# Kernel tuning notes

Hardware: AMD Instinct MI355X
Metric: run time of the kernel (lower is better)

The kernel has to match this reference:

```python
import jax, jax.numpy as jnp
import numpy as np

N_NODES = 100000
N_EDGES = 3200000
F_IN = 256
HEADS = 8
C_OUT = 8
NEG_SLOPE = 0.2


def setup_inputs() -> dict:
    key = jax.random.key(0)
    k1, k2, k3, k4, k5, k6 = jax.random.split(key, 6)
    x = jax.random.normal(k1, (N_NODES, F_IN), dtype=jnp.float32)
    edge_index = jax.random.randint(k2, (2, N_EDGES), 0, N_NODES, dtype=jnp.int64)
    W = jax.random.normal(k3, (F_IN, HEADS * C_OUT), dtype=jnp.float32) * (1.0 / np.sqrt(F_IN))
    att_src = jax.random.normal(k4, (HEADS, C_OUT), dtype=jnp.float32) * 0.1
    att_dst = jax.random.normal(k5, (HEADS, C_OUT), dtype=jnp.float32) * 0.1
    bias = jax.random.normal(k6, (HEADS * C_OUT,), dtype=jnp.float32) * 0.01
    return {"x": x, "edge_index": edge_index, "W": W, "att_src": att_src, "att_dst": att_dst, "bias": bias}


def reference(x, edge_index, W, att_src, att_dst, bias):
    # GATConv (PyG semantics), concat=True, inference (dropout off).
    N = x.shape[0]
    H, C = att_src.shape
    h = (x @ W).reshape(N, H, C)                      # [N,H,C] transformed features
    a_src = jnp.einsum('nhc,hc->nh', h, att_src)      # [N,H]
    a_dst = jnp.einsum('nhc,hc->nh', h, att_dst)      # [N,H]
    src, dst = edge_index[0], edge_index[1]
    # per-edge raw attention logits
    e = jax.nn.leaky_relu(a_src[src] + a_dst[dst], NEG_SLOPE)  # [E,H]
    # segment softmax over incoming edges of each destination node
    m = jax.ops.segment_max(e, dst, num_segments=N)            # [N,H]
    e = jnp.exp(e - m[dst])
    s = jax.ops.segment_sum(e, dst, num_segments=N)            # [N,H]
    alpha = e / (s[dst] + 1e-16)                               # [E,H]
    # scatter-add weighted neighbor features
    out = jax.ops.segment_sum(alpha[:, :, None] * h[src], dst, num_segments=N)  # [N,H,C]
    return out.reshape(N, H * C) + bias
```

## Files before the change

kernel.cpp:

```cpp
#include <hip/hip_runtime.h>
#include <hip/hip_fp16.h>
#include <math.h>

#define F_IN 256
#define HC 64
#define NHEAD 8
#define NEG 0.2f
#define BSH 7
#define BSZ 128
#define CAP 5376
#define HCAP 2944

typedef __attribute__((ext_vector_type(8))) short bf16x8;
typedef __attribute__((ext_vector_type(4))) float f32x4;

union BV { uint4 q; bf16x8 v; };

__device__ __forceinline__ unsigned int hi_pair(float a, float b) {
  return __builtin_amdgcn_perm(__float_as_uint(a), __float_as_uint(b), 0x03020706u);
}
__device__ __forceinline__ unsigned int lo_pair(float a, float b) {
  float ra = a - __uint_as_float(__float_as_uint(a) & 0xffff0000u);
  float rb = b - __uint_as_float(__float_as_uint(b) & 0xffff0000u);
  return __builtin_amdgcn_perm(__float_as_uint(ra), __float_as_uint(rb), 0x03020706u);
}

__global__ __launch_bounds__(256) void k_prep(const float* __restrict__ W,
                                              unsigned short* __restrict__ Wp,
                                              int* __restrict__ bcursor, int NB) {
  int b = blockIdx.x, t = threadIdx.x;
  if (b >= 64) {
    int i = (b - 64) * 256 + t;
    if (i < NB) bcursor[i] = 0;
    return;
  }
  int idx = b * 256 + t;
  int k = idx >> 6, c = idx & 63;
  float w = W[idx];
  unsigned int u = __float_as_uint(w);
  unsigned short hi = (unsigned short)((u + 0x7fffu + ((u >> 16) & 1u)) >> 16);
  float r = w - __uint_as_float((unsigned int)hi << 16);
  unsigned int ur = __float_as_uint(r);
  unsigned short lo = (unsigned short)((ur + 0x7fffu + ((ur >> 16) & 1u)) >> 16);
  int ks = k >> 5, j = k & 7, lg = (k >> 3) & 3;
  int lane = lg * 16 + (c & 15), cg = c >> 4;
  int off = ((ks * 4 + cg) * 64 + lane) * 8 + j;
  Wp[off] = hi;
  Wp[16384 + off] = lo;
}

__global__ __launch_bounds__(512, 4) void k_fused(
    const float* __restrict__ x, const uint4* __restrict__ Wp4,
    const float* __restrict__ att_src, const float* __restrict__ att_dst,
    __half2* __restrict__ h2, float* __restrict__ asrc, float* __restrict__ adst,
    const int* __restrict__ edge, int* __restrict__ bcursor,
    unsigned int* __restrict__ entries, int N, int E, int NB, int NG, int NP) {
  __shared__ __align__(16) unsigned long long srt8[8192];
  __shared__ int hist[1024];
  __shared__ int loff[1024];
  __shared__ int basearr[1024];
  __shared__ int pr[512];
  int b = blockIdx.x;
  int mn = min(NG, NP), m2 = 2 * mn;
  int type, idx;
  if (b < m2) { type = b & 1; idx = b >> 1; }
  else { type = (NG > NP) ? 0 : 1; idx = mn + (b - m2); }
  int t = threadIdx.x;

  if (type == 0) {
    int wv = t >> 6, l = t & 63;
    int lr = l & 15, lg = l >> 4;
    int r0blk = idx * 256;
    char* xb = (char*)srt8;

    float as4[4], ad4[4];
#pragma unroll
    for (int cg = 0; cg < 4; cg++) {
      as4[cg] = att_src[cg * 16 + lr];
      ad4[cg] = att_dst[cg * 16 + lr];
    }
    const uint4* wp = Wp4 + l;

    f32x4 acc[2][4];
#pragma unroll
    for (int i = 0; i < 2; i++)
#pragma unroll
      for (int j = 0; j < 4; j++) acc[i][j] = (f32x4){0.f, 0.f, 0.f, 0.f};

#define STAGE(ks_, buf_)                                                        \
    {                                                                           \
      _Pragma("unroll")                                                         \
      for (int rd = 0; rd < 4; rd++) {                                          \
        int Lbase = rd * 512 + wv * 64;                                         \
        int L = Lbase + l;                                                      \
        int r_ = L >> 3;                                                        \
        int g_ = (L & 7) ^ (r_ & 7);                                            \
        int grow = r0blk + r_; if (grow > N - 1) grow = N - 1;                  \
        __builtin_amdgcn_global_load_lds(                                       \
            (const void*)(x + (size_t)grow * F_IN + (ks_) * 32 + g_ * 4),       \
            (void*)(xb + (buf_) * 32768 + (size_t)Lbase * 16), 16, 0, 0);       \
      }                                                                         \
    }

    STAGE(0, 0);
    __syncthreads();
    int ra_t = wv * 32 + lr, rb_t = ra_t + 16;
    int s0 = ra_t * 8 + ((lg * 2 + 0) ^ (ra_t & 7));
    int s1 = ra_t * 8 + ((lg * 2 + 1) ^ (ra_t & 7));
    int s2 = rb_t * 8 + ((lg * 2 + 0) ^ (rb_t & 7));
    int s3 = rb_t * 8 + ((lg * 2 + 1) ^ (rb_t & 7));

#pragma unroll
    for (int ks = 0; ks < 8; ks++) {
      if (ks < 7) STAGE(ks + 1, (ks + 1) & 1);
      const char* cb = xb + (ks & 1) * 32768;
      float4 p0 = *(const float4*)(cb + (size_t)s0 * 16);
      float4 q0 = *(const float4*)(cb + (size_t)s1 * 16);
      float4 p1 = *(const float4*)(cb + (size_t)s2 * 16);
      float4 q1 = *(const float4*)(cb + (size_t)s3 * 16);
      BV bh[4], bl[4];
#pragma unroll
      for (int cg = 0; cg < 4; cg++) {
        bh[cg].q = wp[(ks * 4 + cg) * 64];
        bl[cg].q = wp[2048 + (ks * 4 + cg) * 64];
      }
      BV ah0, al0, ah1, al1;
      ah0.q.x = hi_pair(p0.x, p0.y); ah0.q.y = hi_pair(p0.z, p0.w);
      ah0.q.z = hi_pair(q0.x, q0.y); ah0.q.w = hi_pair(q0.z, q0.w);
      al0.q.x = lo_pair(p0.x, p0.y); al0.q.y = lo_pair(p0.z, p0.w);
      al0.q.z = lo_pair(q0.x, q0.y); al0.q.w = lo_pair(q0.z, q0.w);
      ah1.q.x = hi_pair(p1.x, p1.y); ah1.q.y = hi_pair(p1.z, p1.w);
      ah1.q.z = hi_pair(q1.x, q1.y); ah1.q.w = hi_pair(q1.z, q1.w);
      al1.q.x = lo_pair(p1.x, p1.y); al1.q.y = lo_pair(p1.z, p1.w);
      al1.q.z = lo_pair(q1.x, q1.y); al1.q.w = lo_pair(q1.z, q1.w);
#pragma unroll
      for (int cg = 0; cg < 4; cg++) {
        acc[0][cg] = __builtin_amdgcn_mfma_f32_16x16x32_bf16(ah0.v, bh[cg].v, acc[0][cg], 0, 0, 0);
        acc[0][cg] = __builtin_amdgcn_mfma_f32_16x16x32_bf16(al0.v, bh[cg].v, acc[0][cg], 0, 0, 0);
        acc[0][cg] = __builtin_amdgcn_mfma_f32_16x16x32_bf16(ah0.v, bl[cg].v, acc[0][cg], 0, 0, 0);
        acc[1][cg] = __builtin_amdgcn_mfma_f32_16x16x32_bf16(ah1.v, bh[cg].v, acc[1][cg], 0, 0, 0);
        acc[1][cg] = __builtin_amdgcn_mfma_f32_16x16x32_bf16(al1.v, bh[cg].v, acc[1][cg], 0, 0, 0);
        acc[1][cg] = __builtin_amdgcn_mfma_f32_16x16x32_bf16(ah1.v, bl[cg].v, acc[1][cg], 0, 0, 0);
      }
      __syncthreads();
    }
#undef STAGE

    int r0 = r0blk + wv * 32;
#pragma unroll
    for (int rg = 0; rg < 2; rg++) {
#pragma unroll
      for (int tt = 0; tt < 4; tt++) {
        int node = r0 + rg * 16 + 4 * lg + tt;
        bool ok = node < N;
        float v0 = acc[rg][0][tt], v1 = acc[rg][1][tt], v2 = acc[rg][2][tt], v3 = acc[rg][3][tt];
        float o0 = __shfl_xor(v0, 1), o1 = __shfl_xor(v1, 1);
        float o2 = __shfl_xor(v2, 1), o3 = __shfl_xor(v3, 1);
        if (ok && !(l & 1)) {
          size_t hb = (size_t)node * 32 + (lr >> 1);
          h2[hb]      = __halves2half2(__float2half_rn(v0), __float2half_rn(o0));
          h2[hb + 8]  = __halves2half2(__float2half_rn(v1), __float2half_rn(o1));
          h2[hb + 16] = __halves2half2(__float2half_rn(v2), __float2half_rn(o2));
          h2[hb + 24] = __halves2half2(__float2half_rn(v3), __float2half_rn(o3));
        }
#pragma unroll
        for (int cg = 0; cg < 4; cg++) {
          float v = (cg == 0) ? v0 : (cg == 1) ? v1 : (cg == 2) ? v2 : v3;
          float s = v * as4[cg];
          float d = v * ad4[cg];
          s += __shfl_xor(s, 1); d += __shfl_xor(d, 1);
          s += __shfl_xor(s, 2); d += __shfl_xor(d, 2);
          s += __shfl_xor(s, 4); d += __shfl_xor(d, 4);
          if (ok && !(l & 7)) {
            int hd = 2 * cg + (lr >> 3);
            asrc[node * NHEAD + hd] = s;
            adst[node * NHEAD + hd] = d;
          }
        }
      }
    }
    return;
  }

  int base = idx * 8192;
  int cblk = min(8192, E - base);
  for (int i = t; i < 1024; i += 512) hist[i] = 0;
  __syncthreads();
#pragma unroll
  for (int j = 0; j < 16; j++) {
    int e = base + j * 512 + t;
    if (e < E) atomicAdd(&hist[edge[E + e] >> BSH], 1);
  }
  __syncthreads();
  int a = hist[2 * t], bb = hist[2 * t + 1];
  pr[t] = a + bb;
  __syncthreads();
  for (int off = 1; off < 512; off <<= 1) {
    int add = (t >= off) ? pr[t - off] : 0;
    __syncthreads();
    pr[t] += add;
    __syncthreads();
  }
  int excl = pr[t] - (a + bb);
  loff[2 * t] = excl;
  loff[2 * t + 1] = excl + a;
  if (a > 0 && 2 * t < NB) basearr[2 * t] = atomicAdd(&bcursor[2 * t], a);
  if (bb > 0 && 2 * t + 1 < NB) basearr[2 * t + 1] = atomicAdd(&bcursor[2 * t + 1], bb);
  hist[2 * t] = excl;
  hist[2 * t + 1] = excl + a;
  __syncthreads();
#pragma unroll
  for (int j = 0; j < 16; j++) {
    int e = base + j * 512 + t;
    if (e < E) {
      int s = edge[e], d = edge[E + e];
      int p = atomicAdd(&hist[d >> BSH], 1);
      srt8[p] = ((unsigned long long)(unsigned int)d << 32) | (unsigned int)s;
    }
  }
  __syncthreads();
  for (int i = t; i < cblk; i += 512) {
    unsigned long long v = srt8[i];
    int d = (int)(v >> 32), s = (int)(v & 0xFFFFFFFFu);
    int bk = d >> BSH;
    int local = basearr[bk] + (i - loff[bk]);
    if (local < CAP)
      entries[(size_t)bk * CAP + local] = ((unsigned int)(d & (BSZ - 1)) << 17) | (unsigned int)s;
  }
}

__global__ __launch_bounds__(512, 6) void k_bagg(
    const unsigned int* __restrict__ entries, const int* __restrict__ bcursor,
    const __half2* __restrict__ h2, const float* __restrict__ asrc,
    const float* __restrict__ adst, const float* __restrict__ bias,
    float* __restrict__ out, int N) {
  __shared__ int srt[HCAP];
  __shared__ int hist[64];
  __shared__ int cur[64];
  __shared__ int off[65];
  int t = threadIdx.x;
  int bkt = blockIdx.x >> 1;
  int hf = blockIdx.x & 1;
  int n0 = (bkt << BSH) + (hf << 6);
  int ncnt = min(64, N - n0);
  if (ncnt <= 0) return;
  int cnt = bcursor[bkt];
  if (cnt > CAP) cnt = CAP;
  const unsigned int* ebase = entries + (size_t)bkt * CAP;
  if (t < 64) hist[t] = 0;
  __syncthreads();
  unsigned int ev[11];
#pragma unroll
  for (int j = 0; j < 11; j++) {
    int i = t + j * 512;
    ev[j] = (i < cnt) ? ebase[i] : 0xFFFFFFFFu;
  }
#pragma unroll
  for (int j = 0; j < 11; j++) {
    int d = (int)(ev[j] >> 17);
    if ((d >> 6) == hf) atomicAdd(&hist[d & 63], 1);
  }
  __syncthreads();
  if (t < 64) {
    int orig = hist[t];
    int v = orig;
#pragma unroll
    for (int o = 1; o < 64; o <<= 1) {
      int u = __shfl_up(v, o);
      if (t >= o) v += u;
    }
    off[t] = v - orig;
    cur[t] = v - orig;
    if (t == 63) off[64] = v;
  }
  __syncthreads();
#pragma unroll
  for (int j = 0; j < 11; j++) {
    unsigned int v = ev[j];
    int d = (int)(v >> 17);
    if ((d >> 6) == hf) {
      int p = atomicAdd(&cur[d & 63], 1);
      if (p < HCAP) srt[p] = (int)(v & 0x1FFFF);
    }
  }
  __syncthreads();
  int wv = t >> 6, l = t & 63;
  int eslot = l >> 3, cg = l & 7;
  for (int nd = wv; nd < ncnt; nd += 8) {
    int node = n0 + nd;
    int sbeg = min(off[nd], HCAP), send = min(off[nd + 1], HCAP);
    float ad = adst[node * NHEAD + cg];
    float a0 = 0.f, a1 = 0.f, a2 = 0.f, a3 = 0.f;
    float a4 = 0.f, a5 = 0.f, a6 = 0.f, a7 = 0.f;
    float wsum = 0.f;
    for (int k = sbeg; k < send; k += 8) {
      int idx = k + eslot;
      bool val = idx < send;
      int s = srt[val ? idx : send - 1];
      float lg = asrc[s * NHEAD + cg] + ad;
      float w = __expf(fmaxf(lg, NEG * lg));
      w = val ? w : 0.f;
      union { uint4 q; __half2 h[4]; } u;
      u.q = *((const uint4*)(h2 + (size_t)s * 32) + cg);
      float2 f0 = __half22float2(u.h[0]);
      float2 f1 = __half22float2(u.h[1]);
      float2 f2 = __half22float2(u.h[2]);
      float2 f3 = __half22float2(u.h[3]);
      a0 = fmaf(w, f0.x, a0); a1 = fmaf(w, f0.y, a1);
      a2 = fmaf(w, f1.x, a2); a3 = fmaf(w, f1.y, a3);
      a4 = fmaf(w, f2.x, a4); a5 = fmaf(w, f2.y, a5);
      a6 = fmaf(w, f3.x, a6); a7 = fmaf(w, f3.y, a7);
      wsum += w;
    }
#pragma unroll
    for (int m = 8; m < 64; m <<= 1) {
      a0 += __shfl_xor(a0, m); a1 += __shfl_xor(a1, m);
      a2 += __shfl_xor(a2, m); a3 += __shfl_xor(a3, m);
      a4 += __shfl_xor(a4, m); a5 += __shfl_xor(a5, m);
      a6 += __shfl_xor(a6, m); a7 += __shfl_xor(a7, m);
      wsum += __shfl_xor(wsum, m);
    }
    if (l < 8) {
      float inv = wsum > 0.f ? 1.0f / wsum : 0.f;
      float4 b0 = *(const float4*)&bias[cg * 8];
      float4 b1 = *(const float4*)&bias[cg * 8 + 4];
      float4 r0, r1;
      r0.x = fmaf(a0, inv, b0.x); r0.y = fmaf(a1, inv, b0.y);
      r0.z = fmaf(a2, inv, b0.z); r0.w = fmaf(a3, inv, b0.w);
      r1.x = fmaf(a4, inv, b1.x); r1.y = fmaf(a5, inv, b1.y);
      r1.z = fmaf(a6, inv, b1.z); r1.w = fmaf(a7, inv, b1.w);
      *(float4*)&out[(size_t)node * HC + cg * 8] = r0;
      *(float4*)&out[(size_t)node * HC + cg * 8 + 4] = r1;
    }
  }
}

extern "C" void kernel_launch(void* const* d_in, const int* in_sizes, int n_in,
                              void* d_out, int out_size, void* d_ws, size_t ws_size,
                              hipStream_t stream) {
  const float* x = (const float*)d_in[0];
  const int* edge = (const int*)d_in[1];
  const float* W = (const float*)d_in[2];
  const float* att_src = (const float*)d_in[3];
  const float* att_dst = (const float*)d_in[4];
  const float* bias = (const float*)d_in[5];
  int N = in_sizes[0] / F_IN;
  int E = in_sizes[1] / 2;
  float* out = (float*)d_out;
  int NB = (N + BSZ - 1) >> BSH;

  unsigned short* Wp = (unsigned short*)d_ws;
  __half2* h2 = (__half2*)((char*)d_ws + 65536);
  float* asrc = (float*)(h2 + (size_t)N * 32);
  float* adst = asrc + (size_t)N * NHEAD;
  int* bcursor = (int*)(adst + (size_t)N * NHEAD);
  unsigned int* entries = (unsigned int*)(bcursor + ((NB + 3) & ~3));

  int NG = (N + 255) / 256;
  int NP = (E + 8191) / 8192;
  int nzb = (NB + 255) / 256;

  k_prep<<<64 + nzb, 256, 0, stream>>>(W, Wp, bcursor, NB);
  k_fused<<<NG + NP, 512, 0, stream>>>(x, (const uint4*)Wp, att_src, att_dst,
                                       h2, asrc, adst, edge, bcursor, entries,
                                       N, E, NB, NG, NP);
  k_bagg<<<2 * NB, 512, 0, stream>>>(entries, bcursor, h2, asrc, adst, bias, out, N);
}
```

Baseline: 299.0 us.

## Use per-wave LDS staging for x tiles and drop block barriers

```diff
diff --git a/kernel.cpp b/kernel.cpp
--- a/kernel.cpp
+++ b/kernel.cpp
@@ -71,7 +71,7 @@
     int wv = t >> 6, l = t & 63;
     int lr = l & 15, lg = l >> 4;
     int r0blk = idx * 256;
-    char* xb = (char*)srt8;
+    char* wb = (char*)srt8 + wv * 8192;
 
     float as4[4], ad4[4];
 #pragma unroll
@@ -91,39 +91,44 @@
     {                                                                           \
       _Pragma("unroll")                                                         \
       for (int rd = 0; rd < 4; rd++) {                                          \
-        int Lbase = rd * 512 + wv * 64;                                         \
-        int L = Lbase + l;                                                      \
-        int r_ = L >> 3;                                                        \
-        int g_ = (L & 7) ^ (r_ & 7);                                            \
-        int grow = r0blk + r_; if (grow > N - 1) grow = N - 1;                  \
+        int r_ = rd * 8 + (l >> 3);                                             \
+        int g_ = (l & 7) ^ (r_ & 7);                                            \
+        int grow = r0blk + wv * 32 + r_; if (grow > N - 1) grow = N - 1;        \
         __builtin_amdgcn_global_load_lds(                                       \
             (const void*)(x + (size_t)grow * F_IN + (ks_) * 32 + g_ * 4),       \
-            (void*)(xb + (buf_) * 32768 + (size_t)Lbase * 16), 16, 0, 0);       \
+            (void*)(wb + (buf_) * 4096 + rd * 1024), 16, 0, 0);                 \
       }                                                                         \
     }
 
     STAGE(0, 0);
-    __syncthreads();
-    int ra_t = wv * 32 + lr, rb_t = ra_t + 16;
-    int s0 = ra_t * 8 + ((lg * 2 + 0) ^ (ra_t & 7));
-    int s1 = ra_t * 8 + ((lg * 2 + 1) ^ (ra_t & 7));
-    int s2 = rb_t * 8 + ((lg * 2 + 0) ^ (rb_t & 7));
-    int s3 = rb_t * 8 + ((lg * 2 + 1) ^ (rb_t & 7));
+    int row_a = lr, row_b = lr + 16;
+    int s0 = row_a * 8 + ((lg * 2 + 0) ^ (row_a & 7));
+    int s1 = row_a * 8 + ((lg * 2 + 1) ^ (row_a & 7));
+    int s2 = row_b * 8 + ((lg * 2 + 0) ^ (row_b & 7));
+    int s3 = row_b * 8 + ((lg * 2 + 1) ^ (row_b & 7));
 
 #pragma unroll
     for (int ks = 0; ks < 8; ks++) {
-      if (ks < 7) STAGE(ks + 1, (ks + 1) & 1);
-      const char* cb = xb + (ks & 1) * 32768;
+      BV bh[4], bl[4];
+#pragma unroll
+      for (int cg = 0; cg < 4; cg++) {
+        bh[cg].q = wp[(ks * 4 + cg) * 64];
+        bl[cg].q = wp[2048 + (ks * 4 + cg) * 64];
+      }
+      __builtin_amdgcn_sched_barrier(0);
+      if (ks < 7) {
+        STAGE(ks + 1, (ks + 1) & 1);
+        __builtin_amdgcn_sched_barrier(0);
+        asm volatile("s_waitcnt vmcnt(12)" ::: "memory");
+      } else {
+        asm volatile("s_waitcnt vmcnt(8)" ::: "memory");
+      }
+      __builtin_amdgcn_sched_barrier(0);
+      const char* cb = wb + (ks & 1) * 4096;
       float4 p0 = *(const float4*)(cb + (size_t)s0 * 16);
       float4 q0 = *(const float4*)(cb + (size_t)s1 * 16);
       float4 p1 = *(const float4*)(cb + (size_t)s2 * 16);
       float4 q1 = *(const float4*)(cb + (size_t)s3 * 16);
-      BV bh[4], bl[4];
-#pragma unroll
-      for (int cg = 0; cg < 4; cg++) {
-        bh[cg].q = wp[(ks * 4 + cg) * 64];
-        bl[cg].q = wp[2048 + (ks * 4 + cg) * 64];
-      }
       BV ah0, al0, ah1, al1;
       ah0.q.x = hi_pair(p0.x, p0.y); ah0.q.y = hi_pair(p0.z, p0.w);
       ah0.q.z = hi_pair(q0.x, q0.y); ah0.q.w = hi_pair(q0.z, q0.w);
@@ -142,7 +147,6 @@
         acc[1][cg] = __builtin_amdgcn_mfma_f32_16x16x32_bf16(al1.v, bh[cg].v, acc[1][cg], 0, 0, 0);
         acc[1][cg] = __builtin_amdgcn_mfma_f32_16x16x32_bf16(ah1.v, bl[cg].v, acc[1][cg], 0, 0, 0);
       }
-      __syncthreads();
     }
 #undef STAGE
 
```

After: 312.7 us. +4.6%, slower.
